# Optimization experiments

Hardware: AMD Instinct MI355X
Metric: run time of the kernel (lower is better)

Reference implementation:

```python
import jax, jax.numpy as jnp
import numpy as np

H, KD, VD = 8, 64, 64
W = 1.25  # custom weight scale


def layer_norm(x, g, b, eps=1e-5):
    m = x.mean(-1, keepdims=True)
    v = ((x - m) ** 2).mean(-1, keepdims=True)
    return (x - m) * jax.lax.rsqrt(v + eps) * g + b


def cross_attention(x1, x2, wq, wk, wv, wo, bo, wm):
    # Conv1d kernel_size=1 == matmul; channel axis splits as (heads, dim)
    b, s1, _ = x1.shape
    s2 = x2.shape[1]
    q = (x1 @ wq.T).reshape(b, s1, H, KD).transpose(0, 2, 1, 3)  # bhqk
    k = (x2 @ wk.T).reshape(b, s2, H, KD).transpose(0, 2, 1, 3)
    v = (x2 @ wv.T).reshape(b, s2, H, VD).transpose(0, 2, 1, 3)
    attn = jnp.einsum('bhqd,bhsd->bhqs', q, k) * (1.0 / (KD ** 0.5))
    attn = jax.nn.softmax(attn * wm, axis=-1)  # elementwise weight BEFORE softmax
    o = jnp.einsum('bhqs,bhsv->bhqv', attn, v)
    o = o.transpose(0, 2, 1, 3).reshape(b, s1, H * VD)
    return o @ wo.T + bo


def make_wm1(nvars, sl2, patch_num):
    sl = sl2 // 2
    wm = jnp.ones((nvars, sl2), jnp.float32)
    wm = wm.at[:2 * patch_num, :sl].multiply(W)
    wm = wm.at[2 * patch_num:, sl:].multiply(W)
    return wm[None, None]  # broadcast over batch, heads


def make_wm2(nvars, sv, patch_num, patch_num_v):
    wm = jnp.ones((nvars, sv), jnp.float32)
    wm = wm.at[:patch_num, :patch_num_v].multiply(W)
    wm = wm.at[patch_num:2 * patch_num, patch_num_v:2 * patch_num_v].multiply(W)
    wm = wm.at[2 * patch_num:, 2 * patch_num_v:].multiply(W)
    return wm[None, None]


def forward(cords_features, spatial_features, speed_features,
            wq1, wk1, wv1, wo1, bo1, wq2, wk2, wv2, wo2, bo2,
            ln1_g, ln1_b, ln2_g, ln2_b, ln3_g, ln3_b,
            ffn_w1, ffn_b1, ffn_w2, ffn_b2):
    b, nvars, d = cords_features.shape
    patch_num = nvars // 3
    patch_num_v = speed_features.shape[1] // 3
    wm1 = make_wm1(nvars, spatial_features.shape[1], patch_num)
    wm2 = make_wm2(nvars, 3 * patch_num_v, patch_num, patch_num_v)
    x = cross_attention(cords_features, spatial_features, wq1, wk1, wv1, wo1, bo1, wm1)
    x = layer_norm(x + cords_features, ln1_g, ln1_b)
    r2 = x
    x = cross_attention(x, speed_features, wq2, wk2, wv2, wo2, bo2, wm2)
    x = layer_norm(x + r2, ln2_g, ln2_b)
    r3 = x
    h = jax.nn.gelu(x @ ffn_w1.T + ffn_b1, approximate=False)
    x = h @ ffn_w2.T + ffn_b2
    return layer_norm(x + r3, ln3_g, ln3_b)


def setup_inputs():
    key = jax.random.key(0)
    ks = jax.random.split(key, 16)
    D, DF = 512, 2048
    s = 0.02
    inp = {
        'cords_features': jax.random.normal(ks[0], (8, 768, D), jnp.float32),
        'spatial_features': jax.random.normal(ks[1], (8, 1024, D), jnp.float32),
        'speed_features': jax.random.normal(ks[2], (8, 768, D), jnp.float32),
        'wq1': jax.random.normal(ks[3], (H * KD, D)) * s,
        'wk1': jax.random.normal(ks[4], (H * KD, D)) * s,
        'wv1': jax.random.normal(ks[5], (H * VD, D)) * s,
        'wo1': jax.random.normal(ks[6], (D, H * VD)) * s,
        'bo1': jnp.zeros((D,), jnp.float32),
        'wq2': jax.random.normal(ks[7], (H * KD, D)) * s,
        'wk2': jax.random.normal(ks[8], (H * KD, D)) * s,
        'wv2': jax.random.normal(ks[9], (H * VD, D)) * s,
        'wo2': jax.random.normal(ks[10], (D, H * VD)) * s,
        'bo2': jnp.zeros((D,), jnp.float32),
        'ln1_g': jnp.ones((D,), jnp.float32), 'ln1_b': jnp.zeros((D,), jnp.float32),
        'ln2_g': jnp.ones((D,), jnp.float32), 'ln2_b': jnp.zeros((D,), jnp.float32),
        'ln3_g': jnp.ones((D,), jnp.float32), 'ln3_b': jnp.zeros((D,), jnp.float32),
        'ffn_w1': jax.random.normal(ks[11], (DF, D)) * s,
        'ffn_b1': jnp.zeros((DF,), jnp.float32),
        'ffn_w2': jax.random.normal(ks[12], (D, DF)) * s,
        'ffn_b2': jnp.zeros((D,), jnp.float32),
    }
    return inp


def reference(cords_features, spatial_features, speed_features,
              wq1, wk1, wv1, wo1, bo1, wq2, wk2, wv2, wo2, bo2,
              ln1_g, ln1_b, ln2_g, ln2_b, ln3_g, ln3_b,
              ffn_w1, ffn_b1, ffn_w2, ffn_b2):
    return forward(cords_features, spatial_features, speed_features,
                   wq1, wk1, wv1, wo1, bo1, wq2, wk2, wv2, wo2, bo2,
                   ln1_g, ln1_b, ln2_g, ln2_b, ln3_g, ln3_b,
                   ffn_w1, ffn_b1, ffn_w2, ffn_b2)
```

## Files before the change

### kernel.cpp

```cpp
#include <hip/hip_runtime.h>
#include <hip/hip_bf16.h>


#define LN_EPS 1e-5f
#define WSCALE 1.25f

typedef __attribute__((ext_vector_type(8))) short short8;
typedef __attribute__((ext_vector_type(4))) float floatx4;
typedef unsigned short us;

__device__ __forceinline__ float bf2f(us u) {
    union { unsigned int i; float f; } v; v.i = ((unsigned int)u) << 16; return v.f;
}
__device__ __forceinline__ us f2bf(float f) {
    union { float f; unsigned int i; } v; v.f = f;
    return (us)((v.i + 0x7FFFu + ((v.i >> 16) & 1u)) >> 16);
}
__device__ __forceinline__ float gelu_f(float v) {
    float x  = v * 0.70710678118654752f;
    float ax = fabsf(x);
    float t  = 1.0f / (1.0f + 0.3275911f * ax);
    float p  = t * (0.254829592f + t * (-0.284496736f + t * (1.421413741f +
               t * (-1.453152027f + t * 1.061405429f))));
    float er = 1.0f - p * __expf(-ax * ax);
    er = copysignf(er, x);
    return 0.5f * v * (1.0f + er);
}

__device__ __forceinline__ int xcd_swizzle_lid()
{
    int nwg = gridDim.x * gridDim.y;
    int lid = blockIdx.y * gridDim.x + blockIdx.x;
    int cpx = nwg >> 3;
    return (lid & 7) * cpx + (lid >> 3);
}

struct CastArgs {
    const float* src[13];
    us* dst[13];
    int blk_ofs[14];
};
__global__ __launch_bounds__(256) void cast_all(CastArgs a)
{
    int b = blockIdx.x;
    int e = 0;
    while (b >= a.blk_ofs[e + 1]) ++e;
    int i = ((b - a.blk_ofs[e]) * 256 + threadIdx.x) * 8;
    const float* s = a.src[e];
    us* d = a.dst[e];
    float4 x = *(const float4*)(s + i);
    float4 y = *(const float4*)(s + i + 4);
    *(ushort4*)(d + i)     = make_ushort4(f2bf(x.x), f2bf(x.y), f2bf(x.z), f2bf(x.w));
    *(ushort4*)(d + i + 4) = make_ushort4(f2bf(y.x), f2bf(y.y), f2bf(y.z), f2bf(y.w));
}

__global__ __launch_bounds__(256) void gemm_r64(
    const us* __restrict__ A, const us* __restrict__ Bw,
    const float* __restrict__ bias, us* __restrict__ Cb,
    int M, int N, int K, int flags)
{
    constexpr int BM = 128, BN = 64;
    constexpr int SLOT = (BM + BN) * 64;
    __shared__ us L[3 * SLOT];

    int t = threadIdx.x;
    int wave = t >> 6, lane = t & 63;

    int swz = xcd_swizzle_lid();
    int gx = gridDim.x;
    int m0 = (swz / gx) * BM, n0 = (swz % gx) * BN;

    int wr = wave * 32;

    int r_in = lane >> 3, pq = lane & 7;
    const us* gA[4]; int lA[4];
#pragma unroll
    for (int c = 0; c < 4; ++c) {
        int r = 32 * c + 8 * wave + r_in;
        int q = pq ^ (r & 7);
        gA[c] = A + (size_t)(m0 + r) * K + 8 * q;
        lA[c] = (32 * c + 8 * wave) * 64;
    }
    const us* gB[2]; int lB[2];
#pragma unroll
    for (int c = 0; c < 2; ++c) {
        int r = 32 * c + 8 * wave + r_in;
        int q = pq ^ (r & 7);
        gB[c] = Bw + (size_t)(n0 + r) * K + 8 * q;
        lB[c] = BM * 64 + (32 * c + 8 * wave) * 64;
    }

    int fcol = lane & 15, fj = lane >> 4;
    int aoff[2][2], boff[4][2];
#pragma unroll
    for (int mt = 0; mt < 2; ++mt)
#pragma unroll
        for (int kc = 0; kc < 2; ++kc) {
            int fr = wr + 16 * mt + fcol;
            aoff[mt][kc] = fr * 64 + ((kc * 4 + fj) ^ (fr & 7)) * 8;
        }
#pragma unroll
    for (int nt = 0; nt < 4; ++nt)
#pragma unroll
        for (int kc = 0; kc < 2; ++kc) {
            int br = 16 * nt + fcol;
            boff[nt][kc] = BM * 64 + br * 64 + ((kc * 4 + fj) ^ (br & 7)) * 8;
        }

    floatx4 acc[2][4] = {};

    auto stage_p0 = [&](int slot, int kt) {
        us* base = L + slot * SLOT;
#pragma unroll
        for (int c = 0; c < 3; ++c)
            __builtin_amdgcn_global_load_lds(
                (const __attribute__((address_space(1))) void*)(gA[c] + (size_t)kt * 64),
                (__attribute__((address_space(3))) void*)(base + lA[c]), 16, 0, 0);
    };
    auto stage_p1 = [&](int slot, int kt) {
        us* base = L + slot * SLOT;
        __builtin_amdgcn_global_load_lds(
            (const __attribute__((address_space(1))) void*)(gA[3] + (size_t)kt * 64),
            (__attribute__((address_space(3))) void*)(base + lA[3]), 16, 0, 0);
#pragma unroll
        for (int c = 0; c < 2; ++c)
            __builtin_amdgcn_global_load_lds(
                (const __attribute__((address_space(1))) void*)(gB[c] + (size_t)kt * 64),
                (__attribute__((address_space(3))) void*)(base + lB[c]), 16, 0, 0);
    };

    int ktrips = K >> 6;
    stage_p0(0, 0); stage_p1(0, 0);
    if (ktrips > 1) {
        stage_p0(1, 1); stage_p1(1, 1);
        asm volatile("s_waitcnt vmcnt(6)" ::: "memory");
    } else {
        asm volatile("s_waitcnt vmcnt(0)" ::: "memory");
    }
    __builtin_amdgcn_s_barrier();
    asm volatile("" ::: "memory");

    int cs = 0;
    for (int tt = 0; tt < ktrips; ++tt) {
        int ns = cs + 2; if (ns >= 3) ns -= 3;
        bool pre = (tt + 2) < ktrips;
        const us* base = L + cs * SLOT;

        if (pre) stage_p0(ns, tt + 2);
        {
            short8 af[2], bfv[4];
#pragma unroll
            for (int mt = 0; mt < 2; ++mt) af[mt] = *(const short8*)(base + aoff[mt][0]);
#pragma unroll
            for (int nt = 0; nt < 4; ++nt) bfv[nt] = *(const short8*)(base + boff[nt][0]);
            __builtin_amdgcn_s_setprio(1);
#pragma unroll
            for (int mt = 0; mt < 2; ++mt)
#pragma unroll
                for (int nt = 0; nt < 4; ++nt)
                    acc[mt][nt] = __builtin_amdgcn_mfma_f32_16x16x32_bf16(
                        af[mt], bfv[nt], acc[mt][nt], 0, 0, 0);
            __builtin_amdgcn_s_setprio(0);
        }

        if (pre) stage_p1(ns, tt + 2);
        {
            short8 af[2], bfv[4];
#pragma unroll
            for (int mt = 0; mt < 2; ++mt) af[mt] = *(const short8*)(base + aoff[mt][1]);
#pragma unroll
            for (int nt = 0; nt < 4; ++nt) bfv[nt] = *(const short8*)(base + boff[nt][1]);
            __builtin_amdgcn_s_setprio(1);
#pragma unroll
            for (int mt = 0; mt < 2; ++mt)
#pragma unroll
                for (int nt = 0; nt < 4; ++nt)
                    acc[mt][nt] = __builtin_amdgcn_mfma_f32_16x16x32_bf16(
                        af[mt], bfv[nt], acc[mt][nt], 0, 0, 0);
            __builtin_amdgcn_s_setprio(0);
        }

        if (tt + 1 < ktrips) {
            if (pre) asm volatile("s_waitcnt vmcnt(6)" ::: "memory");
            else     asm volatile("s_waitcnt vmcnt(0)" ::: "memory");
            __builtin_amdgcn_s_barrier();
            asm volatile("" ::: "memory");
        }
        cs = cs + 1; if (cs >= 3) cs = 0;
    }

    int rq = lane >> 4;
#pragma unroll
    for (int mt = 0; mt < 2; ++mt)
#pragma unroll
        for (int nt = 0; nt < 4; ++nt) {
            int col = n0 + 16 * nt + fcol;
            float bv = (flags & 1) ? bias[col] : 0.f;
#pragma unroll
            for (int r = 0; r < 4; ++r) {
                int row = m0 + wr + 16 * mt + rq * 4 + r;
                float v = acc[mt][nt][r] + bv;
                if (flags & 2) v = gelu_f(v);
                Cb[(size_t)row * N + col] = f2bf(v);
            }
        }
}

template<int BM, int BN>
__global__ __launch_bounds__(512, 2) void gemm_ring(
    const us* __restrict__ A, const us* __restrict__ Bw,
    const float* __restrict__ bias, us* __restrict__ Cb,
    int M, int N, int K, int flags, int vS, us* __restrict__ Vtg)
{
    static_assert(BM == 256 && BN == 128, "gemm_ring fixed at 256x128");
    constexpr int SLOT = (BM + BN) * 64;
    __shared__ us L[3 * SLOT];

    int t = threadIdx.x;
    int wave = t >> 6, lane = t & 63;

    int swz = xcd_swizzle_lid();
    int gx = gridDim.x;
    int m0 = (swz / gx) * BM, n0 = (swz % gx) * BN;

    int wr = (wave >> 1) * 64, wc = (wave & 1) * 64;

    int r_in = lane >> 3, pq = lane & 7;
    const us* gA[4]; int lA[4];
#pragma unroll
    for (int c = 0; c < 4; ++c) {
        int r = 64 * c + 8 * wave + r_in;
        int q = pq ^ (r & 7);
        gA[c] = A + (size_t)(m0 + r) * K + 8 * q;
        lA[c] = (64 * c + 8 * wave) * 64;
    }
    const us* gB[2]; int lB[2];
#pragma unroll
    for (int c = 0; c < 2; ++c) {
        int r = 64 * c + 8 * wave + r_in;
        int q = pq ^ (r & 7);
        gB[c] = Bw + (size_t)(n0 + r) * K + 8 * q;
        lB[c] = BM * 64 + (64 * c + 8 * wave) * 64;
    }

    int fcol = lane & 15, fj = lane >> 4;
    int aoff[4][2], boff[4][2];
#pragma unroll
    for (int mt = 0; mt < 4; ++mt)
#pragma unroll
        for (int kc = 0; kc < 2; ++kc) {
            int fr = wr + 16 * mt + fcol;
            aoff[mt][kc] = fr * 64 + ((kc * 4 + fj) ^ (fr & 7)) * 8;
        }
#pragma unroll
    for (int nt = 0; nt < 4; ++nt)
#pragma unroll
        for (int kc = 0; kc < 2; ++kc) {
            int br = wc + 16 * nt + fcol;
            boff[nt][kc] = BM * 64 + br * 64 + ((kc * 4 + fj) ^ (br & 7)) * 8;
        }

    floatx4 acc[4][4] = {};

    auto stage_p0 = [&](int slot, int kt) {
        us* base = L + slot * SLOT;
#pragma unroll
        for (int c = 0; c < 3; ++c)
            __builtin_amdgcn_global_load_lds(
                (const __attribute__((address_space(1))) void*)(gA[c] + (size_t)kt * 64),
                (__attribute__((address_space(3))) void*)(base + lA[c]), 16, 0, 0);
    };
    auto stage_p1 = [&](int slot, int kt) {
        us* base = L + slot * SLOT;
        __builtin_amdgcn_global_load_lds(
            (const __attribute__((address_space(1))) void*)(gA[3] + (size_t)kt * 64),
            (__attribute__((address_space(3))) void*)(base + lA[3]), 16, 0, 0);
#pragma unroll
        for (int c = 0; c < 2; ++c)
            __builtin_amdgcn_global_load_lds(
                (const __attribute__((address_space(1))) void*)(gB[c] + (size_t)kt * 64),
                (__attribute__((address_space(3))) void*)(base + lB[c]), 16, 0, 0);
    };

    int ktrips = K >> 6;
    stage_p0(0, 0); stage_p1(0, 0);
    if (ktrips > 1) {
        stage_p0(1, 1); stage_p1(1, 1);
        asm volatile("s_waitcnt vmcnt(6)" ::: "memory");
    } else {
        asm volatile("s_waitcnt vmcnt(0)" ::: "memory");
    }
    __builtin_amdgcn_s_barrier();
    asm volatile("" ::: "memory");

    int cs = 0;
    for (int tt = 0; tt < ktrips; ++tt) {
        int ns = cs + 2; if (ns >= 3) ns -= 3;
        bool pre = (tt + 2) < ktrips;
        const us* base = L + cs * SLOT;

        if (pre) stage_p0(ns, tt + 2);
        {
            short8 af[4], bfv[4];
#pragma unroll
            for (int mt = 0; mt < 4; ++mt) af[mt] = *(const short8*)(base + aoff[mt][0]);
#pragma unroll
            for (int nt = 0; nt < 4; ++nt) bfv[nt] = *(const short8*)(base + boff[nt][0]);
            __builtin_amdgcn_s_setprio(1);
#pragma unroll
            for (int mt = 0; mt < 4; ++mt)
#pragma unroll
                for (int nt = 0; nt < 4; ++nt)
                    acc[mt][nt] = __builtin_amdgcn_mfma_f32_16x16x32_bf16(
                        af[mt], bfv[nt], acc[mt][nt], 0, 0, 0);
            __builtin_amdgcn_s_setprio(0);
        }

        if (pre) stage_p1(ns, tt + 2);
        {
            short8 af[4], bfv[4];
#pragma unroll
            for (int mt = 0; mt < 4; ++mt) af[mt] = *(const short8*)(base + aoff[mt][1]);
#pragma unroll
            for (int nt = 0; nt < 4; ++nt) bfv[nt] = *(const short8*)(base + boff[nt][1]);
            __builtin_amdgcn_s_setprio(1);
#pragma unroll
            for (int mt = 0; mt < 4; ++mt)
#pragma unroll
                for (int nt = 0; nt < 4; ++nt)
                    acc[mt][nt] = __builtin_amdgcn_mfma_f32_16x16x32_bf16(
                        af[mt], bfv[nt], acc[mt][nt], 0, 0, 0);
            __builtin_amdgcn_s_setprio(0);
        }

        if (tt + 1 < ktrips) {
            if (pre) asm volatile("s_waitcnt vmcnt(6)" ::: "memory");
            else     asm volatile("s_waitcnt vmcnt(0)" ::: "memory");
            __builtin_amdgcn_s_barrier();
            asm volatile("" ::: "memory");
        }
        cs = cs + 1; if (cs >= 3) cs = 0;
    }

    int rq = lane >> 4;
    if (flags & 8) {
        int b = m0 / vS;
        int s_base = m0 - b * vS;
        if (n0 < 512) {
#pragma unroll
            for (int mt = 0; mt < 4; ++mt)
#pragma unroll
                for (int nt = 0; nt < 4; ++nt) {
                    int col = n0 + wc + 16 * nt + fcol;
#pragma unroll
                    for (int r = 0; r < 4; ++r) {
                        int rloc = wr + 16 * mt + rq * 4 + r;
                        Cb[(size_t)(m0 + rloc) * 512 + col] = f2bf(acc[mt][nt][r]);
                    }
                }
        } else {
#pragma unroll
            for (int mt = 0; mt < 4; ++mt)
#pragma unroll
                for (int nt = 0; nt < 4; ++nt) {
                    int cv = n0 + wc + 16 * nt + fcol - 512;
                    int hv = cv >> 6, dv = cv & 63;
                    int sb = s_base + wr + 16 * mt + rq * 4;
                    ushort4 pk = make_ushort4(
                        f2bf(acc[mt][nt][0]), f2bf(acc[mt][nt][1]),
                        f2bf(acc[mt][nt][2]), f2bf(acc[mt][nt][3]));
                    *(ushort4*)(Vtg + ((size_t)(b * 8 + hv) * 64 + dv) * vS + sb) = pk;
                }
        }
        return;
    }

#pragma unroll
    for (int mt = 0; mt < 4; ++mt)
#pragma unroll
        for (int nt = 0; nt < 4; ++nt) {
            int col = n0 + wc + 16 * nt + fcol;
            float bv = (flags & 1) ? bias[col] : 0.f;
#pragma unroll
            for (int r = 0; r < 4; ++r) {
                int row = m0 + wr + 16 * mt + rq * 4 + r;
                float v = acc[mt][nt][r] + bv;
                if (flags & 2) v = gelu_f(v);
                Cb[(size_t)row * N + col] = f2bf(v);
            }
        }
}

__global__ __launch_bounds__(256, 3) void attn_kernel(
    const us* __restrict__ Q, const us* __restrict__ Kf,
    const us* __restrict__ Vg, us* __restrict__ O,
    int S1, int S2, int shift)
{
    __shared__ us Qs[64 * 64];
    __shared__ us Ks[2][64 * 64];
    __shared__ us Vs[2][64 * 64];
    __shared__ us Ps[64 * 72];

    int t = threadIdx.x;
    int wave = t >> 6, lane = t & 63;
    int quad = lane >> 4, l15 = lane & 15;
    int gid = blockIdx.x & 63;
    int q0 = (blockIdx.x >> 6) * 64;
    int hh = gid & 7, bb = gid >> 3;
    int qb = wave * 16;

    int r_in = lane >> 3, pq = lane & 7;
    const us *gK[2], *gV[2];
    int lofs[2];
#pragma unroll
    for (int c2 = 0; c2 < 2; ++c2) {
        int r = qb + 8 * c2 + r_in;
        int lq = pq ^ (r & 7);
        const us* gQ = Q + ((size_t)bb * S1 + q0 + r) * 512 + hh * 64 + 8 * lq;
        gK[c2] = Kf + ((size_t)bb * S2 + r) * 512 + hh * 64 + 8 * lq;
        gV[c2] = Vg + ((size_t)(bb * 8 + hh) * 64 + r) * S2 + 8 * lq;
        lofs[c2] = (qb + 8 * c2) * 64;
        __builtin_amdgcn_global_load_lds(
            (const __attribute__((address_space(1))) void*)gQ,
            (__attribute__((address_space(3))) void*)(Qs + lofs[c2]), 16, 0, 0);
    }

    int aoffQ[2], poffP[2], boff[4][2];
#pragma unroll
    for (int kc = 0; kc < 2; ++kc) {
        int ph = ((kc * 4 + quad) ^ (l15 & 7)) * 8;
        aoffQ[kc] = (qb + l15) * 64 + ph;
        poffP[kc] = (qb + l15) * 72 + ph;
#pragma unroll
        for (int nt = 0; nt < 4; ++nt)
            boff[nt][kc] = (16 * nt + l15) * 64 + ph;
    }
    int pwoff[4][4];
#pragma unroll
    for (int r = 0; r < 4; ++r) {
        int row = qb + quad * 4 + r;
#pragma unroll
        for (int nt = 0; nt < 4; ++nt) {
            int s = 16 * nt + l15;
            pwoff[nt][r] = row * 72 + (((s >> 3) ^ (row & 7)) * 8) + (s & 7);
        }
    }

    floatx4 acc_o[4] = {};
    float l_part[4] = {0.f, 0.f, 0.f, 0.f};
    int qsh[4];
#pragma unroll
    for (int r = 0; r < 4; ++r) qsh[r] = (q0 + qb + quad * 4 + r) >> shift;

    auto stageKV = [&](int buf, int cc) {
#pragma unroll
        for (int c2 = 0; c2 < 2; ++c2) {
            __builtin_amdgcn_global_load_lds(
                (const __attribute__((address_space(1))) void*)(gK[c2] + (size_t)cc * 512),
                (__attribute__((address_space(3))) void*)(Ks[buf] + lofs[c2]), 16, 0, 0);
            __builtin_amdgcn_global_load_lds(
                (const __attribute__((address_space(1))) void*)(gV[c2] + cc),
                (__attribute__((address_space(3))) void*)(Vs[buf] + lofs[c2]), 16, 0, 0);
        }
    };

    stageKV(0, 0);
    asm volatile("s_waitcnt vmcnt(4)" ::: "memory");
    __builtin_amdgcn_s_barrier();
    asm volatile("" ::: "memory");
    short8 aq0 = *(const short8*)(Qs + aoffQ[0]);
    short8 aq1 = *(const short8*)(Qs + aoffQ[1]);

    int ntile = S2 >> 6;
    for (int ti = 0; ti < ntile; ++ti) {
        int buf = ti & 1;
        if (ti + 1 < ntile) {
            stageKV(buf ^ 1, (ti + 1) << 6);
            asm volatile("s_waitcnt vmcnt(4)" ::: "memory");
        } else {
            asm volatile("s_waitcnt vmcnt(0)" ::: "memory");
        }
        __builtin_amdgcn_s_barrier();
        asm volatile("" ::: "memory");

        const us* ks_ = Ks[buf];
        const us* vs_ = Vs[buf];
        int cbase = ti << 6;

        floatx4 s_acc[4] = {};
#pragma unroll
        for (int nt = 0; nt < 4; ++nt) {
            short8 bk0 = *(const short8*)(ks_ + boff[nt][0]);
            short8 bk1 = *(const short8*)(ks_ + boff[nt][1]);
            s_acc[nt] = __builtin_amdgcn_mfma_f32_16x16x32_bf16(aq0, bk0, s_acc[nt], 0, 0, 0);
            s_acc[nt] = __builtin_amdgcn_mfma_f32_16x16x32_bf16(aq1, bk1, s_acc[nt], 0, 0, 0);
        }

#pragma unroll
        for (int nt = 0; nt < 4; ++nt) {
            int srs = (cbase + 16 * nt + l15) >> shift;
#pragma unroll
            for (int r = 0; r < 4; ++r) {
                float fct = (qsh[r] == srs) ? (0.125f * WSCALE) : 0.125f;
                float p = __expf(s_acc[nt][r] * fct);
                s_acc[nt][r] = p;
                l_part[r] += p;
            }
        }

#pragma unroll
        for (int nt = 0; nt < 4; ++nt)
#pragma unroll
            for (int r = 0; r < 4; ++r)
                Ps[pwoff[nt][r]] = f2bf(s_acc[nt][r]);
        __builtin_amdgcn_wave_barrier();

        short8 ap0 = *(const short8*)(Ps + poffP[0]);
        short8 ap1 = *(const short8*)(Ps + poffP[1]);
#pragma unroll
        for (int nt = 0; nt < 4; ++nt) {
            short8 bv0 = *(const short8*)(vs_ + boff[nt][0]);
            short8 bv1 = *(const short8*)(vs_ + boff[nt][1]);
            acc_o[nt] = __builtin_amdgcn_mfma_f32_16x16x32_bf16(ap0, bv0, acc_o[nt], 0, 0, 0);
            acc_o[nt] = __builtin_amdgcn_mfma_f32_16x16x32_bf16(ap1, bv1, acc_o[nt], 0, 0, 0);
        }

        asm volatile("" ::: "memory");
        __builtin_amdgcn_s_barrier();
    }

#pragma unroll
    for (int r = 0; r < 4; ++r) {
#pragma unroll
        for (int off = 8; off; off >>= 1)
            l_part[r] += __shfl_xor(l_part[r], off, 16);
    }
#pragma unroll
    for (int r = 0; r < 4; ++r) {
        float inv = 1.0f / l_part[r];
        size_t base = ((size_t)bb * S1 + q0 + qb + quad * 4 + r) * 512 + hh * 64;
#pragma unroll
        for (int nt = 0; nt < 4; ++nt)
            O[base + 16 * nt + l15] = f2bf(acc_o[nt][r] * inv);
    }
}

__global__ __launch_bounds__(256) void ln_kernel(
    const us* __restrict__ X, const float* __restrict__ R,
    const float* __restrict__ g, const float* __restrict__ bta,
    float* __restrict__ out, us* __restrict__ outb)
{
    int row = blockIdx.x;
    int t   = threadIdx.x;
    const us*    xr = X + (size_t)row * 512;
    const float* rr = R + (size_t)row * 512;
    float v0 = bf2f(xr[t]) + rr[t];
    float v1 = bf2f(xr[t + 256]) + rr[t + 256];
    float s  = v0 + v1;
    float sq = v0 * v0 + v1 * v1;
#pragma unroll
    for (int off = 32; off; off >>= 1) {
        s  += __shfl_xor(s, off, 64);
        sq += __shfl_xor(sq, off, 64);
    }
    __shared__ float ps[4], psq[4];
    int w = t >> 6;
    if ((t & 63) == 0) { ps[w] = s; psq[w] = sq; }
    __syncthreads();
    float S  = ps[0] + ps[1] + ps[2] + ps[3];
    float SQ = psq[0] + psq[1] + psq[2] + psq[3];
    float mean = S * (1.0f / 512.0f);
    float var  = SQ * (1.0f / 512.0f) - mean * mean;
    float inv  = rsqrtf(var + LN_EPS);
    float y0 = (v0 - mean) * inv * g[t] + bta[t];
    float y1 = (v1 - mean) * inv * g[t + 256] + bta[t + 256];
    out[(size_t)row * 512 + t]       = y0;
    out[(size_t)row * 512 + t + 256] = y1;
    if (outb) {
        outb[(size_t)row * 512 + t]       = f2bf(y0);
        outb[(size_t)row * 512 + t + 256] = f2bf(y1);
    }
}

extern "C" void kernel_launch(void* const* d_in, const int* in_sizes, int n_in,
                              void* d_out, int out_size, void* d_ws, size_t ws_size,
                              hipStream_t stream)
{
    const float* cords   = (const float*)d_in[0];
    const float* spatial = (const float*)d_in[1];
    const float* speed   = (const float*)d_in[2];
    const float* wq1 = (const float*)d_in[3];
    const float* wk1 = (const float*)d_in[4];
    const float* wv1 = (const float*)d_in[5];
    const float* wo1 = (const float*)d_in[6];
    const float* bo1 = (const float*)d_in[7];
    const float* wq2 = (const float*)d_in[8];
    const float* wk2 = (const float*)d_in[9];
    const float* wv2 = (const float*)d_in[10];
    const float* wo2 = (const float*)d_in[11];
    const float* bo2 = (const float*)d_in[12];
    const float* ln1g = (const float*)d_in[13];
    const float* ln1b = (const float*)d_in[14];
    const float* ln2g = (const float*)d_in[15];
    const float* ln2b = (const float*)d_in[16];
    const float* ln3g = (const float*)d_in[17];
    const float* ln3b = (const float*)d_in[18];
    const float* fw1 = (const float*)d_in[19];
    const float* fb1 = (const float*)d_in[20];
    const float* fw2 = (const float*)d_in[21];
    const float* fb2 = (const float*)d_in[22];

    const int B = 8, S1 = 768, S2 = 1024, Sv = 768, D = 512, DF = 2048;
    const int M1 = B * S1;
    const int M2 = B * S2;

    char* w = (char*)d_ws;
    us* q_bf = (us*)w;              w += (size_t)M1 * D * 2;
    us* k_bf = (us*)w;              w += (size_t)M2 * D * 2;
    us* vt   = (us*)w;              w += (size_t)M2 * D * 2;
    us* o_bf = (us*)w;              w += (size_t)M1 * D * 2;
    us* p_bf = (us*)w;              w += (size_t)M1 * D * 2;
    float* x1 = (float*)w;          w += (size_t)M1 * D * 4;
    us* cords_bf   = (us*)w;        w += (size_t)M1 * D * 2;
    us* spatial_bf = (us*)w;        w += (size_t)M2 * D * 2;
    us* speed_bf   = (us*)w;        w += (size_t)M1 * D * 2;
    us* wq1b = (us*)w;              w += (size_t)D * D * 2;
    us* wk1b = (us*)w;              w += (size_t)D * D * 2;
    us* wv1b = (us*)w;              w += (size_t)D * D * 2;
    us* wo1b = (us*)w;              w += (size_t)D * D * 2;
    us* wq2b = (us*)w;              w += (size_t)D * D * 2;
    us* wk2b = (us*)w;              w += (size_t)D * D * 2;
    us* wv2b = (us*)w;              w += (size_t)D * D * 2;
    us* wo2b = (us*)w;              w += (size_t)D * D * 2;
    us* fw1b = (us*)w;              w += (size_t)DF * D * 2;
    us* fw2b = (us*)w;              w += (size_t)DF * D * 2;

    us* h_bf  = q_bf;
    us* y_bf  = p_bf;
    us* x1_bf = spatial_bf;
    us* x2_bf = cords_bf;
    float* x2 = (float*)d_out;

    dim3 blk(256);
    dim3 blk512(512);

    {
        CastArgs ca;
        const float* srcs[13] = {cords, spatial, speed, wq1, wk1, wv1, wo1,
                                 wq2, wk2, wv2, wo2, fw1, fw2};
        us* dsts[13] = {cords_bf, spatial_bf, speed_bf, wq1b, wk1b, wv1b, wo1b,
                        wq2b, wk2b, wv2b, wo2b, fw1b, fw2b};
        int ns[13] = {M1 * D, M2 * D, M1 * D, D * D, D * D, D * D, D * D,
                      D * D, D * D, D * D, D * D, DF * D, DF * D};
        int ofs = 0;
        for (int i = 0; i < 13; ++i) {
            ca.src[i] = srcs[i]; ca.dst[i] = dsts[i];
            ca.blk_ofs[i] = ofs; ofs += ns[i] / 2048;
        }
        ca.blk_ofs[13] = ofs;
        cast_all<<<dim3(ofs), blk, 0, stream>>>(ca);
    }

    auto gr64  = [](int M, int N) { return dim3(N / 64,  M / 128); };
    auto gring = [](int M, int N) { return dim3(N / 128, M / 256); };

    gemm_r64<<<gr64(M1, D), blk, 0, stream>>>(cords_bf, wq1b, nullptr, q_bf, M1, D, D, 0);
    gemm_ring<256, 128><<<gring(M2, 1024), blk512, 0, stream>>>(spatial_bf, wk1b, nullptr, k_bf,
                                                                M2, 1024, D, 8, S2, vt);
    attn_kernel<<<dim3((S1 / 64) * 64), blk, 0, stream>>>(q_bf, k_bf, vt, o_bf, S1, S2, 9);
    gemm_r64<<<gr64(M1, D), blk, 0, stream>>>(o_bf, wo1b, bo1, p_bf, M1, D, D, 1);
    ln_kernel<<<M1, blk, 0, stream>>>(p_bf, cords, ln1g, ln1b, x1, x1_bf);

    gemm_r64<<<gr64(M1, D), blk, 0, stream>>>(x1_bf, wq2b, nullptr, q_bf, M1, D, D, 0);
    gemm_ring<256, 128><<<gring(M1, 1024), blk512, 0, stream>>>(speed_bf, wk2b, nullptr, k_bf,
                                                                M1, 1024, D, 8, Sv, vt);
    attn_kernel<<<dim3((S1 / 64) * 64), blk, 0, stream>>>(q_bf, k_bf, vt, o_bf, S1, Sv, 8);
    gemm_r64<<<gr64(M1, D), blk, 0, stream>>>(o_bf, wo2b, bo2, p_bf, M1, D, D, 1);
    ln_kernel<<<M1, blk, 0, stream>>>(p_bf, x1, ln2g, ln2b, x2, x2_bf);

    gemm_ring<256, 128><<<gring(M1, DF), blk512, 0, stream>>>(x2_bf, fw1b, fb1, h_bf,
                                                              M1, DF, D, 1 | 2 | 4, 0, nullptr);
    gemm_r64<<<gr64(M1, D), blk, 0, stream>>>(h_bf, fw2b, fb2, y_bf, M1, D, DF, 1);
    ln_kernel<<<M1, blk, 0, stream>>>(y_bf, x2, ln3g, ln3b, (float*)d_out, nullptr);

    (void)in_sizes; (void)n_in; (void)out_size; (void)ws_size;
}
```

Before: 331.9 us.

## Batch independent K/V and Q projections into one grouped GEMM launch

Adds a grouped GEMM kernel that computes the layer-1 K/V projection, the layer-2 K/V projection and the layer-1 Q projection in a single launch, with a swizzled block-to-tile mapping. The layer-2 K/V results go to new workspace buffers so they can be produced ahead of time. This removes two launches and fills the GPU better than small separate GEMMs. In exchange it uses more workspace and hardcodes problem sizes (K=512, fixed tile counts, 544 blocks).

```diff
diff --git a/kernel.cpp b/kernel.cpp
--- a/kernel.cpp
+++ b/kernel.cpp
@@ -387,6 +387,204 @@
                 float v = acc[mt][nt][r] + bv;
                 if (flags & 2) v = gelu_f(v);
                 Cb[(size_t)row * N + col] = f2bf(v);
+            }
+        }
+}
+
+__global__ __launch_bounds__(512, 2) void gemm_ring3(
+    const us* __restrict__ A1, const us* __restrict__ B1,
+    us* __restrict__ K1o, us* __restrict__ V1o,
+    const us* __restrict__ A2, const us* __restrict__ B2,
+    us* __restrict__ K2o, us* __restrict__ V2o,
+    const us* __restrict__ A3, const us* __restrict__ B3,
+    us* __restrict__ Q3o)
+{
+    constexpr int SLOT = (256 + 128) * 64;
+    __shared__ us L[3 * SLOT];
+
+    int t = threadIdx.x;
+    int wave = t >> 6, lane = t & 63;
+
+    int nwg = gridDim.x;
+    int lid = blockIdx.x;
+    int cpx = nwg >> 3;
+    int swz = (lid & 7) * cpx + (lid >> 3);
+
+    const us* A; const us* Bw;
+    us* Ko; us* Vo;
+    int vS, m0, n0, sub;
+    if (swz < 256) {
+        sub = 0; int l = swz;
+        A = A1; Bw = B1; Ko = K1o; Vo = V1o; vS = 1024;
+        m0 = (l >> 3) * 256; n0 = (l & 7) * 128;
+    } else if (swz < 448) {
+        sub = 1; int l = swz - 256;
+        A = A2; Bw = B2; Ko = K2o; Vo = V2o; vS = 768;
+        m0 = (l >> 3) * 256; n0 = (l & 7) * 128;
+    } else {
+        sub = 2; int l = swz - 448;
+        A = A3; Bw = B3; Ko = Q3o; Vo = nullptr; vS = 0;
+        m0 = (l >> 2) * 256; n0 = (l & 3) * 128;
+    }
+    const int K = 512;
+
+    int wr = (wave >> 1) * 64, wc = (wave & 1) * 64;
+
+    int r_in = lane >> 3, pq = lane & 7;
+    const us* gA[4]; int lA[4];
+#pragma unroll
+    for (int c = 0; c < 4; ++c) {
+        int r = 64 * c + 8 * wave + r_in;
+        int q = pq ^ (r & 7);
+        gA[c] = A + (size_t)(m0 + r) * K + 8 * q;
+        lA[c] = (64 * c + 8 * wave) * 64;
+    }
+    const us* gB[2]; int lB[2];
+#pragma unroll
+    for (int c = 0; c < 2; ++c) {
+        int r = 64 * c + 8 * wave + r_in;
+        int q = pq ^ (r & 7);
+        gB[c] = Bw + (size_t)(n0 + r) * K + 8 * q;
+        lB[c] = 256 * 64 + (64 * c + 8 * wave) * 64;
+    }
+
+    int fcol = lane & 15, fj = lane >> 4;
+    int aoff[4][2], boff[4][2];
+#pragma unroll
+    for (int mt = 0; mt < 4; ++mt)
+#pragma unroll
+        for (int kc = 0; kc < 2; ++kc) {
+            int fr = wr + 16 * mt + fcol;
+            aoff[mt][kc] = fr * 64 + ((kc * 4 + fj) ^ (fr & 7)) * 8;
+        }
+#pragma unroll
+    for (int nt = 0; nt < 4; ++nt)
+#pragma unroll
+        for (int kc = 0; kc < 2; ++kc) {
+            int br = wc + 16 * nt + fcol;
+            boff[nt][kc] = 256 * 64 + br * 64 + ((kc * 4 + fj) ^ (br & 7)) * 8;
+        }
+
+    floatx4 acc[4][4] = {};
+
+    auto stage_p0 = [&](int slot, int kt) {
+        us* base = L + slot * SLOT;
+#pragma unroll
+        for (int c = 0; c < 3; ++c)
+            __builtin_amdgcn_global_load_lds(
+                (const __attribute__((address_space(1))) void*)(gA[c] + (size_t)kt * 64),
+                (__attribute__((address_space(3))) void*)(base + lA[c]), 16, 0, 0);
+    };
+    auto stage_p1 = [&](int slot, int kt) {
+        us* base = L + slot * SLOT;
+        __builtin_amdgcn_global_load_lds(
+            (const __attribute__((address_space(1))) void*)(gA[3] + (size_t)kt * 64),
+            (__attribute__((address_space(3))) void*)(base + lA[3]), 16, 0, 0);
+#pragma unroll
+        for (int c = 0; c < 2; ++c)
+            __builtin_amdgcn_global_load_lds(
+                (const __attribute__((address_space(1))) void*)(gB[c] + (size_t)kt * 64),
+                (__attribute__((address_space(3))) void*)(base + lB[c]), 16, 0, 0);
+    };
+
+    const int ktrips = K >> 6;
+    stage_p0(0, 0); stage_p1(0, 0);
+    stage_p0(1, 1); stage_p1(1, 1);
+    asm volatile("s_waitcnt vmcnt(6)" ::: "memory");
+    __builtin_amdgcn_s_barrier();
+    asm volatile("" ::: "memory");
+
+    int cs = 0;
+    for (int tt = 0; tt < ktrips; ++tt) {
+        int ns = cs + 2; if (ns >= 3) ns -= 3;
+        bool pre = (tt + 2) < ktrips;
+        const us* base = L + cs * SLOT;
+
+        if (pre) stage_p0(ns, tt + 2);
+        {
+            short8 af[4], bfv[4];
+#pragma unroll
+            for (int mt = 0; mt < 4; ++mt) af[mt] = *(const short8*)(base + aoff[mt][0]);
+#pragma unroll
+            for (int nt = 0; nt < 4; ++nt) bfv[nt] = *(const short8*)(base + boff[nt][0]);
+            __builtin_amdgcn_s_setprio(1);
+#pragma unroll
+            for (int mt = 0; mt < 4; ++mt)
+#pragma unroll
+                for (int nt = 0; nt < 4; ++nt)
+                    acc[mt][nt] = __builtin_amdgcn_mfma_f32_16x16x32_bf16(
+                        af[mt], bfv[nt], acc[mt][nt], 0, 0, 0);
+            __builtin_amdgcn_s_setprio(0);
+        }
+
+        if (pre) stage_p1(ns, tt + 2);
+        {
+            short8 af[4], bfv[4];
+#pragma unroll
+            for (int mt = 0; mt < 4; ++mt) af[mt] = *(const short8*)(base + aoff[mt][1]);
+#pragma unroll
+            for (int nt = 0; nt < 4; ++nt) bfv[nt] = *(const short8*)(base + boff[nt][1]);
+            __builtin_amdgcn_s_setprio(1);
+#pragma unroll
+            for (int mt = 0; mt < 4; ++mt)
+#pragma unroll
+                for (int nt = 0; nt < 4; ++nt)
+                    acc[mt][nt] = __builtin_amdgcn_mfma_f32_16x16x32_bf16(
+                        af[mt], bfv[nt], acc[mt][nt], 0, 0, 0);
+            __builtin_amdgcn_s_setprio(0);
+        }
+
+        if (tt + 1 < ktrips) {
+            if (pre) asm volatile("s_waitcnt vmcnt(6)" ::: "memory");
+            else     asm volatile("s_waitcnt vmcnt(0)" ::: "memory");
+            __builtin_amdgcn_s_barrier();
+            asm volatile("" ::: "memory");
+        }
+        cs = cs + 1; if (cs >= 3) cs = 0;
+    }
+
+    int rq = lane >> 4;
+    if (sub < 2) {
+        int b = m0 / vS;
+        int s_base = m0 - b * vS;
+        if (n0 < 512) {
+#pragma unroll
+            for (int mt = 0; mt < 4; ++mt)
+#pragma unroll
+                for (int nt = 0; nt < 4; ++nt) {
+                    int col = n0 + wc + 16 * nt + fcol;
+#pragma unroll
+                    for (int r = 0; r < 4; ++r) {
+                        int rloc = wr + 16 * mt + rq * 4 + r;
+                        Ko[(size_t)(m0 + rloc) * 512 + col] = f2bf(acc[mt][nt][r]);
+                    }
+                }
+        } else {
+#pragma unroll
+            for (int mt = 0; mt < 4; ++mt)
+#pragma unroll
+                for (int nt = 0; nt < 4; ++nt) {
+                    int cv = n0 + wc + 16 * nt + fcol - 512;
+                    int hv = cv >> 6, dv = cv & 63;
+                    int sb = s_base + wr + 16 * mt + rq * 4;
+                    ushort4 pk = make_ushort4(
+                        f2bf(acc[mt][nt][0]), f2bf(acc[mt][nt][1]),
+                        f2bf(acc[mt][nt][2]), f2bf(acc[mt][nt][3]));
+                    *(ushort4*)(Vo + ((size_t)(b * 8 + hv) * 64 + dv) * vS + sb) = pk;
+                }
+        }
+        return;
+    }
+
+#pragma unroll
+    for (int mt = 0; mt < 4; ++mt)
+#pragma unroll
+        for (int nt = 0; nt < 4; ++nt) {
+            int col = n0 + wc + 16 * nt + fcol;
+#pragma unroll
+            for (int r = 0; r < 4; ++r) {
+                int row = m0 + wr + 16 * mt + rq * 4 + r;
+                Ko[(size_t)row * 512 + col] = f2bf(acc[mt][nt][r]);
             }
         }
 }
@@ -634,6 +832,8 @@
     us* wo2b = (us*)w;              w += (size_t)D * D * 2;
     us* fw1b = (us*)w;              w += (size_t)DF * D * 2;
     us* fw2b = (us*)w;              w += (size_t)DF * D * 2;
+    us* k2_bf = (us*)w;             w += (size_t)M1 * D * 2;
+    us* vt2   = (us*)w;             w += (size_t)M1 * D * 2;
 
     us* h_bf  = q_bf;
     us* y_bf  = p_bf;
@@ -664,17 +864,17 @@
     auto gr64  = [](int M, int N) { return dim3(N / 64,  M / 128); };
     auto gring = [](int M, int N) { return dim3(N / 128, M / 256); };
 
-    gemm_r64<<<gr64(M1, D), blk, 0, stream>>>(cords_bf, wq1b, nullptr, q_bf, M1, D, D, 0);
-    gemm_ring<256, 128><<<gring(M2, 1024), blk512, 0, stream>>>(spatial_bf, wk1b, nullptr, k_bf,
-                                                                M2, 1024, D, 8, S2, vt);
+    gemm_ring3<<<dim3(544), blk512, 0, stream>>>(
+        spatial_bf, wk1b, k_bf, vt,
+        speed_bf,   wk2b, k2_bf, vt2,
+        cords_bf,   wq1b, q_bf);
+
     attn_kernel<<<dim3((S1 / 64) * 64), blk, 0, stream>>>(q_bf, k_bf, vt, o_bf, S1, S2, 9);
     gemm_r64<<<gr64(M1, D), blk, 0, stream>>>(o_bf, wo1b, bo1, p_bf, M1, D, D, 1);
     ln_kernel<<<M1, blk, 0, stream>>>(p_bf, cords, ln1g, ln1b, x1, x1_bf);
 
     gemm_r64<<<gr64(M1, D), blk, 0, stream>>>(x1_bf, wq2b, nullptr, q_bf, M1, D, D, 0);
-    gemm_ring<256, 128><<<gring(M1, 1024), blk512, 0, stream>>>(speed_bf, wk2b, nullptr, k_bf,
-                                                                M1, 1024, D, 8, Sv, vt);
-    attn_kernel<<<dim3((S1 / 64) * 64), blk, 0, stream>>>(q_bf, k_bf, vt, o_bf, S1, Sv, 8);
+    attn_kernel<<<dim3((S1 / 64) * 64), blk, 0, stream>>>(q_bf, k2_bf, vt2, o_bf, S1, Sv, 8);
     gemm_r64<<<gr64(M1, D), blk, 0, stream>>>(o_bf, wo2b, bo2, p_bf, M1, D, D, 1);
     ln_kernel<<<M1, blk, 0, stream>>>(p_bf, x1, ln2g, ln2b, x2, x2_bf);
 
```

After: 341.5 us. 1.03x slower.
